# Kernel optimization log

Hardware: AMD Instinct MI355X
Metric: run time of the kernel (lower is better)

The kernel has to match this reference:

```python
import jax, jax.numpy as jnp
import numpy as np

N = 524288
L = 16            # encoding levels
F = 2             # features per level
LOG2_T = 19
T = 2 ** LOG2_T   # hash table size per level
BASE_RES = 16
FINEST = BASE_RES * 2 ** (L - 1)
WIDTH = 64
DENSITY_OUT = 16

# corner offsets of a voxel, i (x) outer, k (z) inner -- matches BOX_OFFSETS
OFFSETS = jnp.array([[i, j, k] for i in (0, 1) for j in (0, 1) for k in (0, 1)], dtype=jnp.int32)  # [8,3]
# primes wrapped to int32 exactly as jax x32 canonicalization does in the original
PRIMES = jnp.asarray(np.array([1, 2654435761, 805459861], dtype=np.int64).astype(np.int32))
_b = np.exp((np.log(FINEST) - np.log(BASE_RES)) / (L - 1))
RESOLUTIONS = jnp.asarray(np.floor(BASE_RES * _b ** np.arange(L)).astype(np.float32))  # [L]


def sh_encode(d):
    """Spherical harmonic encoding, degree 4 -> [N,25], faithful to source coeffs."""
    x, y, z = d[..., 0:1], d[..., 1:2], d[..., 2:3]
    x2, y2, z2 = x * x, y * y, z * z
    xy, xz, yz = x * y, x * z, y * z
    x4, y4 = x2 * x2, y2 * y2
    out = [jnp.full_like(x, 0.5 * np.sqrt(1.0 / np.pi))]
    c1 = 0.5 * np.sqrt(3.0 / np.pi)
    out += [-c1 * y, c1 * z, -c1 * x]
    sub = 0.25 * np.sqrt(5.0 / np.pi)
    v1 = 0.25 * np.sqrt(15.0 / np.pi)
    v2 = 0.5 * np.sqrt(15.0 / np.pi)
    v3 = 0.75 * np.sqrt(5.0 / np.pi)
    out += [v2 * xy, -v2 * yz, v3 * z2 - sub, -v2 * xz, v1 * x2 - v1 * y2]
    w1 = 0.25 * np.sqrt(105.0 / np.pi)
    w2 = 0.5 * np.sqrt(105.0 / np.pi)
    w3 = 0.25 * np.sqrt(35.0 / (2.0 * np.pi))
    w4 = 0.5 * np.sqrt(7.0 / (6.0 * np.pi))
    out += [-w3 * y * (3.0 * x2 - y2), w2 * xy * z, w4 * y * (1.5 - 7.5 * z2),
            1.24392110863372 * z * (1.5 * z2 - 0.5) - 0.497568443453487 * z,
            w4 * x * (1.5 - 7.5 * z2), w1 * z * (x2 - y2), -w3 * x * (x2 - 3.0 * y2)]
    out += [2.5033429417967 * xy * (x2 - y2),
            -1.77013076977993 * yz * (3.0 * x2 - y2),
            0.126156626101008 * xy * (52.5 * z2 - 7.5),
            0.267618617422916 * y * (2.33333333333333 * z * (1.5 - 7.5 * z2) + 4.0 * z),
            1.48099765681286 * z * (1.66666666666667 * z * (1.5 * z2 - 0.5) - 0.666666666666667 * z) - 0.952069922236839 * z2 + 0.317356640745613,
            0.267618617422916 * x * (2.33333333333333 * z * (1.5 - 7.5 * z2) + 4.0 * z),
            0.063078313050504 * (x2 - y2) * (52.5 * z2 - 7.5),
            -1.77013076977993 * xz * (x2 - 3.0 * y2),
            -3.75501441269506 * x2 * y2 + 0.625835735449176 * x4 + 0.625835735449176 * y4]
    return jnp.concatenate(out, axis=-1)  # [N,25]


def hash_grid_encode(x, tables):
    """x: [N,3] in unit cube; tables: [L,T,F] -> [N, L*F]."""
    def level(table, res):
        grid = 1.0 / res                              # box is [0,1]^3
        bl = jnp.floor(x / grid).astype(jnp.int32)    # bottom-left voxel index [N,3]
        w = (x - bl.astype(x.dtype) * grid) / grid    # trilinear weights [N,3]
        idx = bl[:, None, :] + OFFSETS[None]          # [N,8,3]
        h = ((idx[..., 0] * PRIMES[0]) ^ (idx[..., 1] * PRIMES[1]) ^ (idx[..., 2] * PRIMES[2])) % T
        emb = table[h]                                # [N,8,F] gather
        cw = jnp.where(OFFSETS[None].astype(bool), w[:, None, :], 1.0 - w[:, None, :]).prod(-1)  # [N,8]
        return jnp.einsum('ncf,nc->nf', emb, cw)
    feats = jax.vmap(level)(tables, RESOLUTIONS)      # [L,N,F]
    return jnp.transpose(feats, (1, 0, 2)).reshape(x.shape[0], L * F)


def setup_inputs() -> dict:
    key = jax.random.key(0)
    ks = jax.random.split(key, 8)
    position = jax.random.uniform(ks[0], (N, 3), jnp.float32)
    direction = jax.random.normal(ks[1], (N, 3), jnp.float32)
    hash_tables = jax.random.uniform(ks[2], (L, T, F), jnp.float32, -1e-4, 1e-4)
    def dense(k, fan_in, fan_out):
        return (jax.random.normal(k, (fan_in, fan_out), jnp.float32) / np.sqrt(fan_in),
                jnp.zeros((fan_out,), jnp.float32))
    W_d1, b_d1 = dense(ks[3], L * F, WIDTH)
    W_d2, b_d2 = dense(ks[4], WIDTH, DENSITY_OUT)
    W_c1, b_c1 = dense(ks[5], DENSITY_OUT + 25, WIDTH)
    W_c2, b_c2 = dense(ks[6], WIDTH, WIDTH)
    W_c3, b_c3 = dense(ks[7], WIDTH, 3)
    return dict(position=position, direction=direction, hash_tables=hash_tables,
                W_d1=W_d1, b_d1=b_d1, W_d2=W_d2, b_d2=b_d2,
                W_c1=W_c1, b_c1=b_c1, W_c2=W_c2, b_c2=b_c2, W_c3=W_c3, b_c3=b_c3)


def reference(position, direction, hash_tables, W_d1, b_d1, W_d2, b_d2,
              W_c1, b_c1, W_c2, b_c2, W_c3, b_c3):
    enc_pos = hash_grid_encode(position, hash_tables)     # [N,32]
    enc_dir = sh_encode(direction)                        # [N,25]
    y = jax.nn.relu(enc_pos @ W_d1 + b_d1)                # density MLP (1 hidden layer)
    density_out = y @ W_d2 + b_d2                         # [N,16]
    sigma = jax.nn.relu(density_out[:, -1:])              # [N,1]
    h = jnp.concatenate([density_out, enc_dir], axis=-1)  # [N,41]
    h = jax.nn.relu(h @ W_c1 + b_c1)
    h = jax.nn.relu(h @ W_c2 + b_c2)
    rgb = jax.nn.sigmoid(h @ W_c3 + b_c3)                 # [N,3]
    return (rgb, sigma)
```

## Files before the change

### kernel.cpp

```cpp
#include <hip/hip_runtime.h>
#include <math.h>

#define LEVELS 16
#define TBL 524288
#define TMASK (TBL - 1)

typedef short bf16x8 __attribute__((ext_vector_type(8)));
typedef float f32x4  __attribute__((ext_vector_type(4)));
typedef float fvec4  __attribute__((ext_vector_type(4)));
typedef unsigned int uvec4 __attribute__((ext_vector_type(4)));

static __device__ __forceinline__ unsigned short f2bf(float x) {
    unsigned u = __float_as_uint(x);
    u += 0x7fffu + ((u >> 16) & 1u);
    return (unsigned short)(u >> 16);
}
static __device__ __forceinline__ float b2f(unsigned short h) {
    return __uint_as_float(((unsigned)h) << 16);
}

#define SH_BLOCK(sh, dx, dy, dz)                                                          \
    const float x2 = dx * dx, y2 = dy * dy, z2 = dz * dz;                                 \
    const float xy = dx * dy, xz = dx * dz, yz = dy * dz;                                 \
    const float x4 = x2 * x2, y4 = y2 * y2;                                               \
    const float c0  = (float)(0.5 * sqrt(1.0 / M_PI));                                    \
    const float c1  = (float)(0.5 * sqrt(3.0 / M_PI));                                    \
    const float sub = (float)(0.25 * sqrt(5.0 / M_PI));                                   \
    const float v1  = (float)(0.25 * sqrt(15.0 / M_PI));                                  \
    const float v2  = (float)(0.5 * sqrt(15.0 / M_PI));                                   \
    const float v3  = (float)(0.75 * sqrt(5.0 / M_PI));                                   \
    const float w1c = (float)(0.25 * sqrt(105.0 / M_PI));                                 \
    const float w2c = (float)(0.5 * sqrt(105.0 / M_PI));                                  \
    const float w3c = (float)(0.25 * sqrt(35.0 / (2.0 * M_PI)));                          \
    const float w4c = (float)(0.5 * sqrt(7.0 / (6.0 * M_PI)));                            \
    sh[0] = c0;                                                                           \
    sh[1] = -c1 * dy;                                                                     \
    sh[2] =  c1 * dz;                                                                     \
    sh[3] = -c1 * dx;                                                                     \
    sh[4] =  v2 * xy;                                                                     \
    sh[5] = -v2 * yz;                                                                     \
    sh[6] =  v3 * z2 - sub;                                                               \
    sh[7] = -v2 * xz;                                                                     \
    sh[8] =  v1 * x2 - v1 * y2;                                                           \
    sh[9]  = -w3c * dy * (3.0f * x2 - y2);                                                \
    sh[10] =  w2c * xy * dz;                                                              \
    sh[11] =  w4c * dy * (1.5f - 7.5f * z2);                                              \
    sh[12] =  1.24392110863372f * dz * (1.5f * z2 - 0.5f) - 0.497568443453487f * dz;      \
    sh[13] =  w4c * dx * (1.5f - 7.5f * z2);                                              \
    sh[14] =  w1c * dz * (x2 - y2);                                                       \
    sh[15] = -w3c * dx * (x2 - 3.0f * y2);                                                \
    sh[16] =  2.5033429417967f * xy * (x2 - y2);                                          \
    sh[17] = -1.77013076977993f * yz * (3.0f * x2 - y2);                                  \
    sh[18] =  0.126156626101008f * xy * (52.5f * z2 - 7.5f);                              \
    sh[19] =  0.267618617422916f * dy * (2.33333333333333f * dz * (1.5f - 7.5f * z2) + 4.0f * dz); \
    sh[20] =  1.48099765681286f * dz * (1.66666666666667f * dz * (1.5f * z2 - 0.5f) - 0.666666666666667f * dz) \
              - 0.952069922236839f * z2 + 0.317356640745613f;                             \
    sh[21] =  0.267618617422916f * dx * (2.33333333333333f * dz * (1.5f - 7.5f * z2) + 4.0f * dz); \
    sh[22] =  0.063078313050504f * (x2 - y2) * (52.5f * z2 - 7.5f);                       \
    sh[23] = -1.77013076977993f * xz * (x2 - 3.0f * y2);                                  \
    sh[24] = -3.75501441269506f * x2 * y2 + 0.625835735449176f * x4 + 0.625835735449176f * y4;

__global__ __launch_bounds__(256)
void cvt_tables(const float* __restrict__ tables,
                unsigned int* __restrict__ tb16, int total)
{
    const int i = (blockIdx.x * 256 + threadIdx.x) * 4;
    if (i >= total) return;
    const fvec4 a = __builtin_nontemporal_load((const fvec4*)(tables + 2 * (size_t)i));
    const fvec4 b = __builtin_nontemporal_load((const fvec4*)(tables + 2 * (size_t)i) + 1);
    uvec4 o;
    o.x = ((unsigned)f2bf(a.y) << 16) | f2bf(a.x);
    o.y = ((unsigned)f2bf(a.w) << 16) | f2bf(a.z);
    o.z = ((unsigned)f2bf(b.y) << 16) | f2bf(b.x);
    o.w = ((unsigned)f2bf(b.w) << 16) | f2bf(b.z);
    __builtin_nontemporal_store(o, (uvec4*)&tb16[i]);
}

__global__ __launch_bounds__(256)
void ngp_encode_lvl(const float* __restrict__ pos,
                    const unsigned int* __restrict__ tb16,
                    unsigned int* __restrict__ wsp, int n)
{
    const int b = blockIdx.x;
    const int p = b & 7;
    const int h = b >> 14;
    const int l = 2 * p + h;
    const int c = (b & 16383) >> 3;
    const int idx = c * 256 + threadIdx.x;
    if (idx >= n || l >= LEVELS) return;

    const float px = pos[3 * idx + 0];
    const float py = pos[3 * idx + 1];
    const float pz = pos[3 * idx + 2];

    const float resf = (float)(16 << l);
    const float tx = px * resf, ty = py * resf, tz = pz * resf;
    const float fx = floorf(tx), fy = floorf(ty), fz = floorf(tz);
    const float wx = tx - fx, wy = ty - fy, wz = tz - fz;
    const unsigned ix = (unsigned)(int)fx;
    const unsigned iy = (unsigned)(int)fy;
    const unsigned iz = (unsigned)(int)fz;
    const unsigned hy0 = iy * 2654435761u, hy1 = hy0 + 2654435761u;
    const unsigned hz0 = iz * 805459861u,  hz1 = hz0 + 805459861u;
    const unsigned ix1 = ix + 1u;

    const unsigned int* tb = tb16 + (size_t)l * TBL;
    const unsigned hA = hy0 ^ hz0;
    const unsigned hB = hy0 ^ hz1;
    const unsigned hC = hy1 ^ hz0;
    const unsigned hD = hy1 ^ hz1;

    unsigned eA0, eA1, eB0, eB1, eC0, eC1, eD0, eD1;
    if ((ix & 1u) == 0u) {
        const uint2 pA = *(const uint2*)&tb[((ix ^ hA) & TMASK) & ~1u];
        const uint2 pB = *(const uint2*)&tb[((ix ^ hB) & TMASK) & ~1u];
        const uint2 pC = *(const uint2*)&tb[((ix ^ hC) & TMASK) & ~1u];
        const uint2 pD = *(const uint2*)&tb[((ix ^ hD) & TMASK) & ~1u];
        const unsigned sA = hA & 1u, sB = hB & 1u, sC = hC & 1u, sD = hD & 1u;
        eA0 = sA ? pA.y : pA.x;  eA1 = sA ? pA.x : pA.y;
        eB0 = sB ? pB.y : pB.x;  eB1 = sB ? pB.x : pB.y;
        eC0 = sC ? pC.y : pC.x;  eC1 = sC ? pC.x : pC.y;
        eD0 = sD ? pD.y : pD.x;  eD1 = sD ? pD.x : pD.y;
    } else {
        eA0 = tb[(ix  ^ hA) & TMASK];  eA1 = tb[(ix1 ^ hA) & TMASK];
        eB0 = tb[(ix  ^ hB) & TMASK];  eB1 = tb[(ix1 ^ hB) & TMASK];
        eC0 = tb[(ix  ^ hC) & TMASK];  eC1 = tb[(ix1 ^ hC) & TMASK];
        eD0 = tb[(ix  ^ hD) & TMASK];  eD1 = tb[(ix1 ^ hD) & TMASK];
    }

#define UNPX(e) __uint_as_float((e) << 16)
#define UNPY(e) __uint_as_float((e) & 0xffff0000u)

    const float ux = 1.f - wx, uy = 1.f - wy, uz = 1.f - wz;
    const float c000 = ux * uy * uz, c001 = ux * uy * wz;
    const float c010 = ux * wy * uz, c011 = ux * wy * wz;
    const float c100 = wx * uy * uz, c101 = wx * uy * wz;
    const float c110 = wx * wy * uz, c111 = wx * wy * wz;

    float f0 = UNPX(eA0) * c000, f1 = UNPY(eA0) * c000;
    f0 = fmaf(UNPX(eB0), c001, f0); f1 = fmaf(UNPY(eB0), c001, f1);
    f0 = fmaf(UNPX(eC0), c010, f0); f1 = fmaf(UNPY(eC0), c010, f1);
    f0 = fmaf(UNPX(eD0), c011, f0); f1 = fmaf(UNPY(eD0), c011, f1);
    f0 = fmaf(UNPX(eA1), c100, f0); f1 = fmaf(UNPY(eA1), c100, f1);
    f0 = fmaf(UNPX(eB1), c101, f0); f1 = fmaf(UNPY(eB1), c101, f1);
    f0 = fmaf(UNPX(eC1), c110, f0); f1 = fmaf(UNPY(eC1), c110, f1);
    f0 = fmaf(UNPX(eD1), c111, f0); f1 = fmaf(UNPY(eD1), c111, f1);

    const unsigned int h0 = f2bf(f0);
    const unsigned int h1 = f2bf(f1);
    __builtin_nontemporal_store((h1 << 16) | h0, &wsp[(size_t)l * n + idx]);
}

#define MT   512
#define GROUPS 8
#define SW1  32
#define SW   72
#define SA   65
#define OW1  0
#define OW2  2048
#define OC1H 3200
#define OC1L 7808
#define OC2H 12416
#define OC2L 17024
#define OC3H 21632
#define OC3L 22784
#define WTOT 23936

__global__ __launch_bounds__(512, 2)
void ngp_mlp_mfma4(const unsigned int* __restrict__ wsp,
                   const float* __restrict__ dirp,
                   const float* __restrict__ Wd1, const float* __restrict__ bd1,
                   const float* __restrict__ Wd2, const float* __restrict__ bd2,
                   const float* __restrict__ Wc1, const float* __restrict__ bc1,
                   const float* __restrict__ Wc2, const float* __restrict__ bc2,
                   const float* __restrict__ Wc3, const float* __restrict__ bc3,
                   float* __restrict__ out, int n)
{
    __shared__ short wsm[WTOT];
    __shared__ float act[8 * 16 * SA];
    const int tid = threadIdx.x;

    for (int t = tid; t < WTOT; t += MT) wsm[t] = 0;
    __syncthreads();

    for (int g = tid; g < 32 * 64; g += MT) {
        const int k = g >> 6, nn = g & 63;
        wsm[OW1 + nn * SW1 + k] = f2bf(Wd1[g]);
    }
    for (int g = tid; g < 64 * 16; g += MT) {
        const int k = g >> 4, nn = g & 15;
        wsm[OW2 + nn * SW + k] = f2bf(Wd2[g]);
    }
    for (int g = tid; g < 41 * 64; g += MT) {
        const int k = g >> 6, nn = g & 63;
        const float w = Wc1[g];
        const unsigned short hh = f2bf(w);
        wsm[OC1H + nn * SW + k] = hh;
        wsm[OC1L + nn * SW + k] = f2bf(w - b2f(hh));
    }
    for (int g = tid; g < 64 * 64; g += MT) {
        const int k = g >> 6, nn = g & 63;
        const float w = Wc2[g];
        const unsigned short hh = f2bf(w);
        wsm[OC2H + nn * SW + k] = hh;
        wsm[OC2L + nn * SW + k] = f2bf(w - b2f(hh));
    }
    for (int g = tid; g < 64 * 3; g += MT) {
        const int k = g / 3, nn = g - 3 * k;
        const float w = Wc3[g];
        const unsigned short hh = f2bf(w);
        wsm[OC3H + nn * SW + k] = hh;
        wsm[OC3L + nn * SW + k] = f2bf(w - b2f(hh));
    }
    __syncthreads();

    const int wid = tid >> 6;
    const int lane = tid & 63;
    const int ln = lane & 15;
    const int qd = lane >> 4;
    float* A = act + wid * (16 * SA);

    float bd1v[4], bc1v[4], bc2v[4];
#pragma unroll
    for (int t = 0; t < 4; ++t) {
        bd1v[t] = bd1[t * 16 + ln];
        bc1v[t] = bc1[t * 16 + ln];
        bc2v[t] = bc2[t * 16 + ln];
    }
    const float bd2v = bd2[ln];
    const float bc3v = (ln < 3) ? bc3[ln] : 0.f;

#define LOAD_SPLIT(ah, al, k0)                                   \
    {                                                            \
        _Pragma("unroll")                                        \
        for (int j = 0; j < 8; ++j) {                            \
            const float v = A[ln * SA + (k0) + j];               \
            const unsigned short hb = f2bf(v);                   \
            ah[j] = (short)hb;                                   \
            al[j] = (short)f2bf(v - b2f(hb));                    \
        }                                                        \
    }

#define SPLIT_TILE(acc, ah0, ah1, al0, al1, OH, OL, row)                                          \
    {                                                                                             \
        const bf16x8 bh0 = *(const bf16x8*)&wsm[(OH) + (row) * SW + qd * 8];                      \
        const bf16x8 bh1 = *(const bf16x8*)&wsm[(OH) + (row) * SW + 32 + qd * 8];                 \
        acc = __builtin_amdgcn_mfma_f32_16x16x32_bf16(ah0, bh0, acc, 0, 0, 0);                    \
        acc = __builtin_amdgcn_mfma_f32_16x16x32_bf16(ah1, bh1, acc, 0, 0, 0);                    \
        acc = __builtin_amdgcn_mfma_f32_16x16x32_bf16(al0, bh0, acc, 0, 0, 0);                    \
        acc = __builtin_amdgcn_mfma_f32_16x16x32_bf16(al1, bh1, acc, 0, 0, 0);                    \
        const bf16x8 bl0 = *(const bf16x8*)&wsm[(OL) + (row) * SW + qd * 8];                      \
        const bf16x8 bl1 = *(const bf16x8*)&wsm[(OL) + (row) * SW + 32 + qd * 8];                 \
        acc = __builtin_amdgcn_mfma_f32_16x16x32_bf16(ah0, bl0, acc, 0, 0, 0);                    \
        acc = __builtin_amdgcn_mfma_f32_16x16x32_bf16(ah1, bl1, acc, 0, 0, 0);                    \
    }

    const int pt0 = blockIdx.x * (GROUPS * 128) + wid * 16 + ln;
    unsigned int xu0, xu1, xu2, xu3;
    float dq0, dq1, dq2;
    xu0 = wsp[(size_t)(qd * 4 + 0) * n + pt0];
    xu1 = wsp[(size_t)(qd * 4 + 1) * n + pt0];
    xu2 = wsp[(size_t)(qd * 4 + 2) * n + pt0];
    xu3 = wsp[(size_t)(qd * 4 + 3) * n + pt0];
    dq0 = dirp[3 * pt0 + 0];
    dq1 = dirp[3 * pt0 + 1];
    dq2 = dirp[3 * pt0 + 2];

#pragma unroll 1
    for (int grp = 0; grp < GROUPS; ++grp) {
        const int pt_base = blockIdx.x * (GROUPS * 128) + grp * 128 + wid * 16;
        const int pt = pt_base + ln;

        bf16x8 ax;
        ax[0] = (short)(xu0 & 0xffffu); ax[1] = (short)(xu0 >> 16);
        ax[2] = (short)(xu1 & 0xffffu); ax[3] = (short)(xu1 >> 16);
        ax[4] = (short)(xu2 & 0xffffu); ax[5] = (short)(xu2 >> 16);
        ax[6] = (short)(xu3 & 0xffffu); ax[7] = (short)(xu3 >> 16);
        const float ddx = dq0, ddy = dq1, ddz = dq2;

        if (grp + 1 < GROUPS) {
            const int ptn = pt + 128;
            xu0 = wsp[(size_t)(qd * 4 + 0) * n + ptn];
            xu1 = wsp[(size_t)(qd * 4 + 1) * n + ptn];
            xu2 = wsp[(size_t)(qd * 4 + 2) * n + ptn];
            xu3 = wsp[(size_t)(qd * 4 + 3) * n + ptn];
            dq0 = dirp[3 * ptn + 0];
            dq1 = dirp[3 * ptn + 1];
            dq2 = dirp[3 * ptn + 2];
        }

        f32x4 yacc[4];
#pragma unroll
        for (int t = 0; t < 4; ++t) {
            const bf16x8 b = *(const bf16x8*)&wsm[OW1 + (t * 16 + ln) * SW1 + qd * 8];
            const float bv = bd1v[t];
            f32x4 acc = {bv, bv, bv, bv};
            yacc[t] = __builtin_amdgcn_mfma_f32_16x16x32_bf16(ax, b, acc, 0, 0, 0);
        }
#pragma unroll
        for (int t = 0; t < 4; ++t)
#pragma unroll
            for (int r = 0; r < 4; ++r)
                A[(qd * 4 + r) * SA + t * 16 + ln] = fmaxf(yacc[t][r], 0.f);

        {
            bf16x8 a0, a1;
#pragma unroll
            for (int j = 0; j < 8; ++j) a0[j] = (short)f2bf(A[ln * SA + qd * 8 + j]);
#pragma unroll
            for (int j = 0; j < 8; ++j) a1[j] = (short)f2bf(A[ln * SA + 32 + qd * 8 + j]);
            const bf16x8 b0 = *(const bf16x8*)&wsm[OW2 + ln * SW + qd * 8];
            const bf16x8 b1 = *(const bf16x8*)&wsm[OW2 + ln * SW + 32 + qd * 8];
            const float bv = bd2v;
            f32x4 acc = {bv, bv, bv, bv};
            acc = __builtin_amdgcn_mfma_f32_16x16x32_bf16(a0, b0, acc, 0, 0, 0);
            acc = __builtin_amdgcn_mfma_f32_16x16x32_bf16(a1, b1, acc, 0, 0, 0);
            if (ln == 15) {
#pragma unroll
                for (int r = 0; r < 4; ++r)
                    out[3 * n + pt_base + qd * 4 + r] = fmaxf(acc[r], 0.f);
            }
#pragma unroll
            for (int r = 0; r < 4; ++r)
                A[(qd * 4 + r) * SA + ln] = acc[r];
        }

        {
            float sh[25];
            SH_BLOCK(sh, ddx, ddy, ddz)
#pragma unroll
            for (int i = 0; i < 25; ++i)
                if ((i & 3) == qd)
                    A[ln * SA + 16 + i] = sh[i];
        }

        {
            bf16x8 ah0, ah1, al0, al1;
            LOAD_SPLIT(ah0, al0, qd * 8)
            LOAD_SPLIT(ah1, al1, 32 + qd * 8)
            f32x4 hacc[4];
#pragma unroll
            for (int t = 0; t < 4; ++t) {
                const float bv = bc1v[t];
                f32x4 acc = {bv, bv, bv, bv};
                SPLIT_TILE(acc, ah0, ah1, al0, al1, OC1H, OC1L, t * 16 + ln)
                hacc[t] = acc;
            }
#pragma unroll
            for (int t = 0; t < 4; ++t)
#pragma unroll
                for (int r = 0; r < 4; ++r)
                    A[(qd * 4 + r) * SA + t * 16 + ln] = fmaxf(hacc[t][r], 0.f);
        }

        {
            bf16x8 ah0, ah1, al0, al1;
            LOAD_SPLIT(ah0, al0, qd * 8)
            LOAD_SPLIT(ah1, al1, 32 + qd * 8)
            f32x4 hacc[4];
#pragma unroll
            for (int t = 0; t < 4; ++t) {
                const float bv = bc2v[t];
                f32x4 acc = {bv, bv, bv, bv};
                SPLIT_TILE(acc, ah0, ah1, al0, al1, OC2H, OC2L, t * 16 + ln)
                hacc[t] = acc;
            }
#pragma unroll
            for (int t = 0; t < 4; ++t)
#pragma unroll
                for (int r = 0; r < 4; ++r)
                    A[(qd * 4 + r) * SA + t * 16 + ln] = fmaxf(hacc[t][r], 0.f);
        }

        {
            bf16x8 ah0, ah1, al0, al1;
            LOAD_SPLIT(ah0, al0, qd * 8)
            LOAD_SPLIT(ah1, al1, 32 + qd * 8)
            const float bv = bc3v;
            f32x4 acc = {bv, bv, bv, bv};
            SPLIT_TILE(acc, ah0, ah1, al0, al1, OC3H, OC3L, ln)
            if (ln < 3) {
#pragma unroll
                for (int r = 0; r < 4; ++r)
                    out[3 * (pt_base + qd * 4 + r) + ln] = 1.f / (1.f + expf(-acc[r]));
            }
        }
    }
}

__global__ __launch_bounds__(256)
void nerf_fused(const float* __restrict__ pos,
                const float* __restrict__ dirp,
                const float* __restrict__ tables,
                const float* __restrict__ Wd1, const float* __restrict__ bd1,
                const float* __restrict__ Wd2, const float* __restrict__ bd2,
                const float* __restrict__ Wc1, const float* __restrict__ bc1,
                const float* __restrict__ Wc2, const float* __restrict__ bc2,
                const float* __restrict__ Wc3, const float* __restrict__ bc3,
                float* __restrict__ out, int n)
{
    const int idx = blockIdx.x * blockDim.x + threadIdx.x;
    if (idx >= n) return;
    const float px = pos[3 * idx + 0], py = pos[3 * idx + 1], pz = pos[3 * idx + 2];
    float y[64];
#pragma unroll
    for (int j = 0; j < 64; ++j) y[j] = bd1[j];
#pragma unroll
    for (int l = 0; l < LEVELS; ++l) {
        const float resf = (float)(16 << l);
        const float tx = px * resf, ty = py * resf, tz = pz * resf;
        const float fx = floorf(tx), fy = floorf(ty), fz = floorf(tz);
        const float wx = tx - fx, wy = ty - fy, wz = tz - fz;
        const unsigned ix = (unsigned)(int)fx, iy = (unsigned)(int)fy, iz = (unsigned)(int)fz;
        const unsigned hy0 = iy * 2654435761u, hy1 = hy0 + 2654435761u;
        const unsigned hz0 = iz * 805459861u,  hz1 = hz0 + 805459861u;
        const unsigned ix1 = ix + 1u;
        const float2* tb = (const float2*)tables + (size_t)l * TBL;
        const float2 e000 = tb[(ix  ^ hy0 ^ hz0) & TMASK];
        const float2 e001 = tb[(ix  ^ hy0 ^ hz1) & TMASK];
        const float2 e010 = tb[(ix  ^ hy1 ^ hz0) & TMASK];
        const float2 e011 = tb[(ix  ^ hy1 ^ hz1) & TMASK];
        const float2 e100 = tb[(ix1 ^ hy0 ^ hz0) & TMASK];
        const float2 e101 = tb[(ix1 ^ hy0 ^ hz1) & TMASK];
        const float2 e110 = tb[(ix1 ^ hy1 ^ hz0) & TMASK];
        const float2 e111 = tb[(ix1 ^ hy1 ^ hz1) & TMASK];
        const float ux = 1.f - wx, uy = 1.f - wy, uz = 1.f - wz;
        const float c000 = ux*uy*uz, c001 = ux*uy*wz, c010 = ux*wy*uz, c011 = ux*wy*wz;
        const float c100 = wx*uy*uz, c101 = wx*uy*wz, c110 = wx*wy*uz, c111 = wx*wy*wz;
        float f0 = e000.x*c000, f1 = e000.y*c000;
        f0 = fmaf(e001.x,c001,f0); f1 = fmaf(e001.y,c001,f1);
        f0 = fmaf(e010.x,c010,f0); f1 = fmaf(e010.y,c010,f1);
        f0 = fmaf(e011.x,c011,f0); f1 = fmaf(e011.y,c011,f1);
        f0 = fmaf(e100.x,c100,f0); f1 = fmaf(e100.y,c100,f1);
        f0 = fmaf(e101.x,c101,f0); f1 = fmaf(e101.y,c101,f1);
        f0 = fmaf(e110.x,c110,f0); f1 = fmaf(e110.y,c110,f1);
        f0 = fmaf(e111.x,c111,f0); f1 = fmaf(e111.y,c111,f1);
        const float* w0 = Wd1 + (size_t)(2 * l) * 64;
#pragma unroll
        for (int j = 0; j < 64; ++j)
            y[j] = fmaf(f0, w0[j], fmaf(f1, w0[64 + j], y[j]));
    }
    float d[16];
#pragma unroll
    for (int k = 0; k < 16; ++k) d[k] = bd2[k];
#pragma unroll
    for (int j = 0; j < 64; ++j) {
        const float a = fmaxf(y[j], 0.f);
#pragma unroll
        for (int k = 0; k < 16; ++k) d[k] = fmaf(a, Wd2[j * 16 + k], d[k]);
    }
    out[3 * n + idx] = fmaxf(d[15], 0.f);
    const float dx = dirp[3*idx], dy = dirp[3*idx+1], dz = dirp[3*idx+2];
    float sh[25];
    SH_BLOCK(sh, dx, dy, dz)
    float h1[64];
#pragma unroll
    for (int j = 0; j < 64; ++j) h1[j] = bc1[j];
#pragma unroll
    for (int i = 0; i < 16; ++i) {
#pragma unroll
        for (int j = 0; j < 64; ++j) h1[j] = fmaf(d[i], Wc1[i * 64 + j], h1[j]);
    }
#pragma unroll
    for (int s = 0; s < 25; ++s) {
#pragma unroll
        for (int j = 0; j < 64; ++j) h1[j] = fmaf(sh[s], Wc1[(16 + s) * 64 + j], h1[j]);
    }
    float h2[64];
#pragma unroll
    for (int j = 0; j < 64; ++j) h2[j] = bc2[j];
#pragma unroll
    for (int i = 0; i < 64; ++i) {
        const float a = fmaxf(h1[i], 0.f);
#pragma unroll
        for (int j = 0; j < 64; ++j) h2[j] = fmaf(a, Wc2[i * 64 + j], h2[j]);
    }
    float r0 = bc3[0], r1 = bc3[1], r2 = bc3[2];
#pragma unroll
    for (int j = 0; j < 64; ++j) {
        const float a = fmaxf(h2[j], 0.f);
        r0 = fmaf(a, Wc3[j * 3 + 0], r0);
        r1 = fmaf(a, Wc3[j * 3 + 1], r1);
        r2 = fmaf(a, Wc3[j * 3 + 2], r2);
    }
    out[3 * idx + 0] = 1.f / (1.f + expf(-r0));
    out[3 * idx + 1] = 1.f / (1.f + expf(-r1));
    out[3 * idx + 2] = 1.f / (1.f + expf(-r2));
}

extern "C" void kernel_launch(void* const* d_in, const int* in_sizes, int n_in,
                              void* d_out, int out_size, void* d_ws, size_t ws_size,
                              hipStream_t stream) {
    const float* pos    = (const float*)d_in[0];
    const float* dir    = (const float*)d_in[1];
    const float* tables = (const float*)d_in[2];
    const float* Wd1 = (const float*)d_in[3];
    const float* bd1 = (const float*)d_in[4];
    const float* Wd2 = (const float*)d_in[5];
    const float* bd2 = (const float*)d_in[6];
    const float* Wc1 = (const float*)d_in[7];
    const float* bc1 = (const float*)d_in[8];
    const float* Wc2 = (const float*)d_in[9];
    const float* bc2 = (const float*)d_in[10];
    const float* Wc3 = (const float*)d_in[11];
    const float* bc3 = (const float*)d_in[12];

    const int n = in_sizes[0] / 3;
    const int blocks = (n + 255) / 256;

    if (ws_size >= (size_t)n * 128 && n == 524288) {
        unsigned int* wsp  = (unsigned int*)d_ws;
        unsigned int* tb16 = (unsigned int*)((char*)d_ws + (size_t)n * 64);
        const int total = LEVELS * TBL;
        cvt_tables<<<total / 1024, 256, 0, stream>>>(tables, tb16, total);
        ngp_encode_lvl<<<16 * blocks, 256, 0, stream>>>(pos, tb16, wsp, n);
        ngp_mlp_mfma4<<<n / (128 * GROUPS), MT, 0, stream>>>((const unsigned int*)wsp, dir,
                                                             Wd1, bd1, Wd2, bd2,
                                                             Wc1, bc1, Wc2, bc2, Wc3, bc3,
                                                             (float*)d_out, n);
    } else {
        nerf_fused<<<blocks, 256, 0, stream>>>(pos, dir, tables,
                                               Wd1, bd1, Wd2, bd2,
                                               Wc1, bc1, Wc2, bc2, Wc3, bc3,
                                               (float*)d_out, n);
    }
}
```

Baseline: 360.7 us.

## Process two 16-point tiles per wave in MLP and split encode launches

The MLP kernel moves from 512 to 256 threads per block, with each wave now handling two 16-point tiles (A and B) so every B-operand weight fragment loaded from shared memory feeds twice as many MFMAs. It also emits SH coefficients directly into the activation buffer, pads the activation stride from 65 to 68, shrinks the Wc3 weight region (rows indexed by ln&3), and adds sched_barriers between output tiles. The level-encode launch is split into two launches of eight levels each, replacing the old interleaved block-to-level mapping. The costs are higher register pressure per wave, which could hurt occupancy, and one extra kernel launch.

```diff
diff --git a/kernel.cpp b/kernel.cpp
--- a/kernel.cpp
+++ b/kernel.cpp
@@ -60,6 +60,49 @@
     sh[23] = -1.77013076977993f * xz * (x2 - 3.0f * y2);                                  \
     sh[24] = -3.75501441269506f * x2 * y2 + 0.625835735449176f * x4 + 0.625835735449176f * y4;
 
+#define SH_EMIT(Ash, DXV, DYV, DZV)                                                        \
+    {                                                                                      \
+        const float sx2 = (DXV)*(DXV), sy2 = (DYV)*(DYV), sz2 = (DZV)*(DZV);               \
+        const float sxy = (DXV)*(DYV), sxz = (DXV)*(DZV), syz = (DYV)*(DZV);               \
+        const float sx4 = sx2*sx2, sy4 = sy2*sy2;                                          \
+        const float k0  = (float)(0.5 * sqrt(1.0 / M_PI));                                 \
+        const float k1  = (float)(0.5 * sqrt(3.0 / M_PI));                                 \
+        const float ksub= (float)(0.25 * sqrt(5.0 / M_PI));                                \
+        const float kv1 = (float)(0.25 * sqrt(15.0 / M_PI));                               \
+        const float kv2 = (float)(0.5 * sqrt(15.0 / M_PI));                                \
+        const float kv3 = (float)(0.75 * sqrt(5.0 / M_PI));                                \
+        const float kw1 = (float)(0.25 * sqrt(105.0 / M_PI));                              \
+        const float kw2 = (float)(0.5 * sqrt(105.0 / M_PI));                               \
+        const float kw3 = (float)(0.25 * sqrt(35.0 / (2.0 * M_PI)));                       \
+        const float kw4 = (float)(0.5 * sqrt(7.0 / (6.0 * M_PI)));                         \
+        if ((0  & 3) == qd) (Ash)[0]  = k0;                                                \
+        if ((1  & 3) == qd) (Ash)[1]  = -k1 * (DYV);                                       \
+        if ((2  & 3) == qd) (Ash)[2]  =  k1 * (DZV);                                       \
+        if ((3  & 3) == qd) (Ash)[3]  = -k1 * (DXV);                                       \
+        if ((4  & 3) == qd) (Ash)[4]  =  kv2 * sxy;                                        \
+        if ((5  & 3) == qd) (Ash)[5]  = -kv2 * syz;                                        \
+        if ((6  & 3) == qd) (Ash)[6]  =  kv3 * sz2 - ksub;                                 \
+        if ((7  & 3) == qd) (Ash)[7]  = -kv2 * sxz;                                        \
+        if ((8  & 3) == qd) (Ash)[8]  =  kv1 * sx2 - kv1 * sy2;                            \
+        if ((9  & 3) == qd) (Ash)[9]  = -kw3 * (DYV) * (3.0f * sx2 - sy2);                 \
+        if ((10 & 3) == qd) (Ash)[10] =  kw2 * sxy * (DZV);                                \
+        if ((11 & 3) == qd) (Ash)[11] =  kw4 * (DYV) * (1.5f - 7.5f * sz2);                \
+        if ((12 & 3) == qd) (Ash)[12] =  1.24392110863372f * (DZV) * (1.5f * sz2 - 0.5f) - 0.497568443453487f * (DZV); \
+        if ((13 & 3) == qd) (Ash)[13] =  kw4 * (DXV) * (1.5f - 7.5f * sz2);                \
+        if ((14 & 3) == qd) (Ash)[14] =  kw1 * (DZV) * (sx2 - sy2);                        \
+        if ((15 & 3) == qd) (Ash)[15] = -kw3 * (DXV) * (sx2 - 3.0f * sy2);                 \
+        if ((16 & 3) == qd) (Ash)[16] =  2.5033429417967f * sxy * (sx2 - sy2);             \
+        if ((17 & 3) == qd) (Ash)[17] = -1.77013076977993f * syz * (3.0f * sx2 - sy2);     \
+        if ((18 & 3) == qd) (Ash)[18] =  0.126156626101008f * sxy * (52.5f * sz2 - 7.5f);  \
+        if ((19 & 3) == qd) (Ash)[19] =  0.267618617422916f * (DYV) * (2.33333333333333f * (DZV) * (1.5f - 7.5f * sz2) + 4.0f * (DZV)); \
+        if ((20 & 3) == qd) (Ash)[20] =  1.48099765681286f * (DZV) * (1.66666666666667f * (DZV) * (1.5f * sz2 - 0.5f) - 0.666666666666667f * (DZV)) \
+                                         - 0.952069922236839f * sz2 + 0.317356640745613f;  \
+        if ((21 & 3) == qd) (Ash)[21] =  0.267618617422916f * (DXV) * (2.33333333333333f * (DZV) * (1.5f - 7.5f * sz2) + 4.0f * (DZV)); \
+        if ((22 & 3) == qd) (Ash)[22] =  0.063078313050504f * (sx2 - sy2) * (52.5f * sz2 - 7.5f); \
+        if ((23 & 3) == qd) (Ash)[23] = -1.77013076977993f * sxz * (sx2 - 3.0f * sy2);     \
+        if ((24 & 3) == qd) (Ash)[24] = -3.75501441269506f * sx2 * sy2 + 0.625835735449176f * sx4 + 0.625835735449176f * sy4; \
+    }
+
 __global__ __launch_bounds__(256)
 void cvt_tables(const float* __restrict__ tables,
                 unsigned int* __restrict__ tb16, int total)
@@ -79,13 +122,11 @@
 __global__ __launch_bounds__(256)
 void ngp_encode_lvl(const float* __restrict__ pos,
                     const unsigned int* __restrict__ tb16,
-                    unsigned int* __restrict__ wsp, int n)
+                    unsigned int* __restrict__ wsp, int n, int lbase)
 {
     const int b = blockIdx.x;
-    const int p = b & 7;
-    const int h = b >> 14;
-    const int l = 2 * p + h;
-    const int c = (b & 16383) >> 3;
+    const int l = lbase + (b & 7);
+    const int c = b >> 3;
     const int idx = c * 256 + threadIdx.x;
     if (idx >= n || l >= LEVELS) return;
 
@@ -151,11 +192,10 @@
     __builtin_nontemporal_store((h1 << 16) | h0, &wsp[(size_t)l * n + idx]);
 }
 
-#define MT   512
 #define GROUPS 8
 #define SW1  32
 #define SW   72
-#define SA   65
+#define SA   68
 #define OW1  0
 #define OW2  2048
 #define OC1H 3200
@@ -163,10 +203,10 @@
 #define OC2H 12416
 #define OC2L 17024
 #define OC3H 21632
-#define OC3L 22784
-#define WTOT 23936
-
-__global__ __launch_bounds__(512, 2)
+#define OC3L 21920
+#define WTOT 22208
+
+__global__ __launch_bounds__(256, 2)
 void ngp_mlp_mfma4(const unsigned int* __restrict__ wsp,
                    const float* __restrict__ dirp,
                    const float* __restrict__ Wd1, const float* __restrict__ bd1,
@@ -177,35 +217,35 @@
                    float* __restrict__ out, int n)
 {
     __shared__ short wsm[WTOT];
-    __shared__ float act[8 * 16 * SA];
+    __shared__ float act[4 * 32 * SA];
     const int tid = threadIdx.x;
 
-    for (int t = tid; t < WTOT; t += MT) wsm[t] = 0;
+    for (int t = tid; t < WTOT; t += 256) wsm[t] = 0;
     __syncthreads();
 
-    for (int g = tid; g < 32 * 64; g += MT) {
+    for (int g = tid; g < 32 * 64; g += 256) {
         const int k = g >> 6, nn = g & 63;
         wsm[OW1 + nn * SW1 + k] = f2bf(Wd1[g]);
     }
-    for (int g = tid; g < 64 * 16; g += MT) {
+    for (int g = tid; g < 64 * 16; g += 256) {
         const int k = g >> 4, nn = g & 15;
         wsm[OW2 + nn * SW + k] = f2bf(Wd2[g]);
     }
-    for (int g = tid; g < 41 * 64; g += MT) {
+    for (int g = tid; g < 41 * 64; g += 256) {
         const int k = g >> 6, nn = g & 63;
         const float w = Wc1[g];
         const unsigned short hh = f2bf(w);
         wsm[OC1H + nn * SW + k] = hh;
         wsm[OC1L + nn * SW + k] = f2bf(w - b2f(hh));
     }
-    for (int g = tid; g < 64 * 64; g += MT) {
+    for (int g = tid; g < 64 * 64; g += 256) {
         const int k = g >> 6, nn = g & 63;
         const float w = Wc2[g];
         const unsigned short hh = f2bf(w);
         wsm[OC2H + nn * SW + k] = hh;
         wsm[OC2L + nn * SW + k] = f2bf(w - b2f(hh));
     }
-    for (int g = tid; g < 64 * 3; g += MT) {
+    for (int g = tid; g < 64 * 3; g += 256) {
         const int k = g / 3, nn = g - 3 * k;
         const float w = Wc3[g];
         const unsigned short hh = f2bf(w);
@@ -218,7 +258,8 @@
     const int lane = tid & 63;
     const int ln = lane & 15;
     const int qd = lane >> 4;
-    float* A = act + wid * (16 * SA);
+    float* A0 = act + wid * (32 * SA);
+    float* A1 = A0 + 16 * SA;
 
     float bd1v[4], bc1v[4], bc2v[4];
 #pragma unroll
@@ -230,159 +271,199 @@
     const float bd2v = bd2[ln];
     const float bc3v = (ln < 3) ? bc3[ln] : 0.f;
 
-#define LOAD_SPLIT(ah, al, k0)                                   \
+#define LOAD_SPLITP(AP, ah, al, k0)                              \
     {                                                            \
         _Pragma("unroll")                                        \
         for (int j = 0; j < 8; ++j) {                            \
-            const float v = A[ln * SA + (k0) + j];               \
+            const float v = (AP)[ln * SA + (k0) + j];            \
             const unsigned short hb = f2bf(v);                   \
             ah[j] = (short)hb;                                   \
             al[j] = (short)f2bf(v - b2f(hb));                    \
         }                                                        \
     }
 
-#define SPLIT_TILE(acc, ah0, ah1, al0, al1, OH, OL, row)                                          \
+#define SPLIT_TILE2(accA, accB, hA0, hA1, lA0, lA1, hB0, hB1, lB0, lB1, OH, OL, row)              \
     {                                                                                             \
         const bf16x8 bh0 = *(const bf16x8*)&wsm[(OH) + (row) * SW + qd * 8];                      \
         const bf16x8 bh1 = *(const bf16x8*)&wsm[(OH) + (row) * SW + 32 + qd * 8];                 \
-        acc = __builtin_amdgcn_mfma_f32_16x16x32_bf16(ah0, bh0, acc, 0, 0, 0);                    \
-        acc = __builtin_amdgcn_mfma_f32_16x16x32_bf16(ah1, bh1, acc, 0, 0, 0);                    \
-        acc = __builtin_amdgcn_mfma_f32_16x16x32_bf16(al0, bh0, acc, 0, 0, 0);                    \
-        acc = __builtin_amdgcn_mfma_f32_16x16x32_bf16(al1, bh1, acc, 0, 0, 0);                    \
+        accA = __builtin_amdgcn_mfma_f32_16x16x32_bf16(hA0, bh0, accA, 0, 0, 0);                  \
+        accA = __builtin_amdgcn_mfma_f32_16x16x32_bf16(hA1, bh1, accA, 0, 0, 0);                  \
+        accA = __builtin_amdgcn_mfma_f32_16x16x32_bf16(lA0, bh0, accA, 0, 0, 0);                  \
+        accA = __builtin_amdgcn_mfma_f32_16x16x32_bf16(lA1, bh1, accA, 0, 0, 0);                  \
+        accB = __builtin_amdgcn_mfma_f32_16x16x32_bf16(hB0, bh0, accB, 0, 0, 0);                  \
+        accB = __builtin_amdgcn_mfma_f32_16x16x32_bf16(hB1, bh1, accB, 0, 0, 0);                  \
+        accB = __builtin_amdgcn_mfma_f32_16x16x32_bf16(lB0, bh0, accB, 0, 0, 0);                  \
+        accB = __builtin_amdgcn_mfma_f32_16x16x32_bf16(lB1, bh1, accB, 0, 0, 0);                  \
         const bf16x8 bl0 = *(const bf16x8*)&wsm[(OL) + (row) * SW + qd * 8];                      \
         const bf16x8 bl1 = *(const bf16x8*)&wsm[(OL) + (row) * SW + 32 + qd * 8];                 \
-        acc = __builtin_amdgcn_mfma_f32_16x16x32_bf16(ah0, bl0, acc, 0, 0, 0);                    \
-        acc = __builtin_amdgcn_mfma_f32_16x16x32_bf16(ah1, bl1, acc, 0, 0, 0);                    \
-    }
-
-    const int pt0 = blockIdx.x * (GROUPS * 128) + wid * 16 + ln;
-    unsigned int xu0, xu1, xu2, xu3;
-    float dq0, dq1, dq2;
-    xu0 = wsp[(size_t)(qd * 4 + 0) * n + pt0];
-    xu1 = wsp[(size_t)(qd * 4 + 1) * n + pt0];
-    xu2 = wsp[(size_t)(qd * 4 + 2) * n + pt0];
-    xu3 = wsp[(size_t)(qd * 4 + 3) * n + pt0];
-    dq0 = dirp[3 * pt0 + 0];
-    dq1 = dirp[3 * pt0 + 1];
-    dq2 = dirp[3 * pt0 + 2];
+        accA = __builtin_amdgcn_mfma_f32_16x16x32_bf16(hA0, bl0, accA, 0, 0, 0);                  \
+        accA = __builtin_amdgcn_mfma_f32_16x16x32_bf16(hA1, bl1, accA, 0, 0, 0);                  \
+        accB = __builtin_amdgcn_mfma_f32_16x16x32_bf16(hB0, bl0, accB, 0, 0, 0);                  \
+        accB = __builtin_amdgcn_mfma_f32_16x16x32_bf16(hB1, bl1, accB, 0, 0, 0);                  \
+    }
+
+    const int ptA0 = blockIdx.x * (GROUPS * 128) + wid * 32 + ln;
+    unsigned int xuA0, xuA1, xuA2, xuA3, xuB0, xuB1, xuB2, xuB3;
+    float dqA0, dqA1, dqA2, dqB0, dqB1, dqB2;
+    xuA0 = wsp[(size_t)(qd * 4 + 0) * n + ptA0];
+    xuA1 = wsp[(size_t)(qd * 4 + 1) * n + ptA0];
+    xuA2 = wsp[(size_t)(qd * 4 + 2) * n + ptA0];
+    xuA3 = wsp[(size_t)(qd * 4 + 3) * n + ptA0];
+    xuB0 = wsp[(size_t)(qd * 4 + 0) * n + ptA0 + 16];
+    xuB1 = wsp[(size_t)(qd * 4 + 1) * n + ptA0 + 16];
+    xuB2 = wsp[(size_t)(qd * 4 + 2) * n + ptA0 + 16];
+    xuB3 = wsp[(size_t)(qd * 4 + 3) * n + ptA0 + 16];
+    dqA0 = dirp[3 * ptA0 + 0];
+    dqA1 = dirp[3 * ptA0 + 1];
+    dqA2 = dirp[3 * ptA0 + 2];
+    dqB0 = dirp[3 * (ptA0 + 16) + 0];
+    dqB1 = dirp[3 * (ptA0 + 16) + 1];
+    dqB2 = dirp[3 * (ptA0 + 16) + 2];
 
 #pragma unroll 1
     for (int grp = 0; grp < GROUPS; ++grp) {
-        const int pt_base = blockIdx.x * (GROUPS * 128) + grp * 128 + wid * 16;
+        const int pt_base = blockIdx.x * (GROUPS * 128) + grp * 128 + wid * 32;
         const int pt = pt_base + ln;
 
-        bf16x8 ax;
-        ax[0] = (short)(xu0 & 0xffffu); ax[1] = (short)(xu0 >> 16);
-        ax[2] = (short)(xu1 & 0xffffu); ax[3] = (short)(xu1 >> 16);
-        ax[4] = (short)(xu2 & 0xffffu); ax[5] = (short)(xu2 >> 16);
-        ax[6] = (short)(xu3 & 0xffffu); ax[7] = (short)(xu3 >> 16);
-        const float ddx = dq0, ddy = dq1, ddz = dq2;
+        bf16x8 axA, axB;
+        axA[0] = (short)(xuA0 & 0xffffu); axA[1] = (short)(xuA0 >> 16);
+        axA[2] = (short)(xuA1 & 0xffffu); axA[3] = (short)(xuA1 >> 16);
+        axA[4] = (short)(xuA2 & 0xffffu); axA[5] = (short)(xuA2 >> 16);
+        axA[6] = (short)(xuA3 & 0xffffu); axA[7] = (short)(xuA3 >> 16);
+        axB[0] = (short)(xuB0 & 0xffffu); axB[1] = (short)(xuB0 >> 16);
+        axB[2] = (short)(xuB1 & 0xffffu); axB[3] = (short)(xuB1 >> 16);
+        axB[4] = (short)(xuB2 & 0xffffu); axB[5] = (short)(xuB2 >> 16);
+        axB[6] = (short)(xuB3 & 0xffffu); axB[7] = (short)(xuB3 >> 16);
+        const float dAx = dqA0, dAy = dqA1, dAz = dqA2;
+        const float dBx = dqB0, dBy = dqB1, dBz = dqB2;
 
         if (grp + 1 < GROUPS) {
             const int ptn = pt + 128;
-            xu0 = wsp[(size_t)(qd * 4 + 0) * n + ptn];
-            xu1 = wsp[(size_t)(qd * 4 + 1) * n + ptn];
-            xu2 = wsp[(size_t)(qd * 4 + 2) * n + ptn];
-            xu3 = wsp[(size_t)(qd * 4 + 3) * n + ptn];
-            dq0 = dirp[3 * ptn + 0];
-            dq1 = dirp[3 * ptn + 1];
-            dq2 = dirp[3 * ptn + 2];
+            xuA0 = wsp[(size_t)(qd * 4 + 0) * n + ptn];
+            xuA1 = wsp[(size_t)(qd * 4 + 1) * n + ptn];
+            xuA2 = wsp[(size_t)(qd * 4 + 2) * n + ptn];
+            xuA3 = wsp[(size_t)(qd * 4 + 3) * n + ptn];
+            xuB0 = wsp[(size_t)(qd * 4 + 0) * n + ptn + 16];
+            xuB1 = wsp[(size_t)(qd * 4 + 1) * n + ptn + 16];
+            xuB2 = wsp[(size_t)(qd * 4 + 2) * n + ptn + 16];
+            xuB3 = wsp[(size_t)(qd * 4 + 3) * n + ptn + 16];
+            dqA0 = dirp[3 * ptn + 0];
+            dqA1 = dirp[3 * ptn + 1];
+            dqA2 = dirp[3 * ptn + 2];
+            dqB0 = dirp[3 * (ptn + 16) + 0];
+            dqB1 = dirp[3 * (ptn + 16) + 1];
+            dqB2 = dirp[3 * (ptn + 16) + 2];
         }
 
-        f32x4 yacc[4];
 #pragma unroll
         for (int t = 0; t < 4; ++t) {
             const bf16x8 b = *(const bf16x8*)&wsm[OW1 + (t * 16 + ln) * SW1 + qd * 8];
             const float bv = bd1v[t];
-            f32x4 acc = {bv, bv, bv, bv};
-            yacc[t] = __builtin_amdgcn_mfma_f32_16x16x32_bf16(ax, b, acc, 0, 0, 0);
+            f32x4 accA = {bv, bv, bv, bv};
+            f32x4 accB = {bv, bv, bv, bv};
+            accA = __builtin_amdgcn_mfma_f32_16x16x32_bf16(axA, b, accA, 0, 0, 0);
+            accB = __builtin_amdgcn_mfma_f32_16x16x32_bf16(axB, b, accB, 0, 0, 0);
+#pragma unroll
+            for (int r = 0; r < 4; ++r) {
+                A0[(qd * 4 + r) * SA + t * 16 + ln] = fmaxf(accA[r], 0.f);
+                A1[(qd * 4 + r) * SA + t * 16 + ln] = fmaxf(accB[r], 0.f);
+            }
         }
-#pragma unroll
-        for (int t = 0; t < 4; ++t)
-#pragma unroll
-            for (int r = 0; r < 4; ++r)
-                A[(qd * 4 + r) * SA + t * 16 + ln] = fmaxf(yacc[t][r], 0.f);
 
         {
-            bf16x8 a0, a1;
-#pragma unroll
-            for (int j = 0; j < 8; ++j) a0[j] = (short)f2bf(A[ln * SA + qd * 8 + j]);
-#pragma unroll
-            for (int j = 0; j < 8; ++j) a1[j] = (short)f2bf(A[ln * SA + 32 + qd * 8 + j]);
+            bf16x8 a0A, a1A, a0B, a1B;
+#pragma unroll
+            for (int j = 0; j < 8; ++j) a0A[j] = (short)f2bf(A0[ln * SA + qd * 8 + j]);
+#pragma unroll
+            for (int j = 0; j < 8; ++j) a1A[j] = (short)f2bf(A0[ln * SA + 32 + qd * 8 + j]);
+#pragma unroll
+            for (int j = 0; j < 8; ++j) a0B[j] = (short)f2bf(A1[ln * SA + qd * 8 + j]);
+#pragma unroll
+            for (int j = 0; j < 8; ++j) a1B[j] = (short)f2bf(A1[ln * SA + 32 + qd * 8 + j]);
             const bf16x8 b0 = *(const bf16x8*)&wsm[OW2 + ln * SW + qd * 8];
             const bf16x8 b1 = *(const bf16x8*)&wsm[OW2 + ln * SW + 32 + qd * 8];
             const float bv = bd2v;
-            f32x4 acc = {bv, bv, bv, bv};
-            acc = __builtin_amdgcn_mfma_f32_16x16x32_bf16(a0, b0, acc, 0, 0, 0);
-            acc = __builtin_amdgcn_mfma_f32_16x16x32_bf16(a1, b1, acc, 0, 0, 0);
+            f32x4 accA = {bv, bv, bv, bv};
+            f32x4 accB = {bv, bv, bv, bv};
+            accA = __builtin_amdgcn_mfma_f32_16x16x32_bf16(a0A, b0, accA, 0, 0, 0);
+            accA = __builtin_amdgcn_mfma_f32_16x16x32_bf16(a1A, b1, accA, 0, 0, 0);
+            accB = __builtin_amdgcn_mfma_f32_16x16x32_bf16(a0B, b0, accB, 0, 0, 0);
+            accB = __builtin_amdgcn_mfma_f32_16x16x32_bf16(a1B, b1, accB, 0, 0, 0);
             if (ln == 15) {
 #pragma unroll
-                for (int r = 0; r < 4; ++r)
-                    out[3 * n + pt_base + qd * 4 + r] = fmaxf(acc[r], 0.f);
+                for (int r = 0; r < 4; ++r) {
+                    out[3 * n + pt_base + qd * 4 + r]      = fmaxf(accA[r], 0.f);
+                    out[3 * n + pt_base + 16 + qd * 4 + r] = fmaxf(accB[r], 0.f);
+                }
             }
 #pragma unroll
-            for (int r = 0; r < 4; ++r)
-                A[(qd * 4 + r) * SA + ln] = acc[r];
+            for (int r = 0; r < 4; ++r) {
+                A0[(qd * 4 + r) * SA + ln] = accA[r];
+                A1[(qd * 4 + r) * SA + ln] = accB[r];
+            }
         }
 
+        SH_EMIT(&A0[ln * SA + 16], dAx, dAy, dAz)
+        SH_EMIT(&A1[ln * SA + 16], dBx, dBy, dBz)
+
         {
-            float sh[25];
-            SH_BLOCK(sh, ddx, ddy, ddz)
-#pragma unroll
-            for (int i = 0; i < 25; ++i)
-                if ((i & 3) == qd)
-                    A[ln * SA + 16 + i] = sh[i];
-        }
-
-        {
-            bf16x8 ah0, ah1, al0, al1;
-            LOAD_SPLIT(ah0, al0, qd * 8)
-            LOAD_SPLIT(ah1, al1, 32 + qd * 8)
-            f32x4 hacc[4];
+            bf16x8 hA0, hA1, lA0, lA1, hB0, hB1, lB0, lB1;
+            LOAD_SPLITP(A0, hA0, lA0, qd * 8)
+            LOAD_SPLITP(A0, hA1, lA1, 32 + qd * 8)
+            LOAD_SPLITP(A1, hB0, lB0, qd * 8)
+            LOAD_SPLITP(A1, hB1, lB1, 32 + qd * 8)
 #pragma unroll
             for (int t = 0; t < 4; ++t) {
                 const float bv = bc1v[t];
-                f32x4 acc = {bv, bv, bv, bv};
-                SPLIT_TILE(acc, ah0, ah1, al0, al1, OC1H, OC1L, t * 16 + ln)
-                hacc[t] = acc;
+                f32x4 accA = {bv, bv, bv, bv};
+                f32x4 accB = {bv, bv, bv, bv};
+                SPLIT_TILE2(accA, accB, hA0, hA1, lA0, lA1, hB0, hB1, lB0, lB1, OC1H, OC1L, t * 16 + ln)
+#pragma unroll
+                for (int r = 0; r < 4; ++r) {
+                    A0[(qd * 4 + r) * SA + t * 16 + ln] = fmaxf(accA[r], 0.f);
+                    A1[(qd * 4 + r) * SA + t * 16 + ln] = fmaxf(accB[r], 0.f);
+                }
+                __builtin_amdgcn_sched_barrier(0);
             }
-#pragma unroll
-            for (int t = 0; t < 4; ++t)
-#pragma unroll
-                for (int r = 0; r < 4; ++r)
-                    A[(qd * 4 + r) * SA + t * 16 + ln] = fmaxf(hacc[t][r], 0.f);
         }
 
         {
-            bf16x8 ah0, ah1, al0, al1;
-            LOAD_SPLIT(ah0, al0, qd * 8)
-            LOAD_SPLIT(ah1, al1, 32 + qd * 8)
-            f32x4 hacc[4];
+            bf16x8 hA0, hA1, lA0, lA1, hB0, hB1, lB0, lB1;
+            LOAD_SPLITP(A0, hA0, lA0, qd * 8)
+            LOAD_SPLITP(A0, hA1, lA1, 32 + qd * 8)
+            LOAD_SPLITP(A1, hB0, lB0, qd * 8)
+            LOAD_SPLITP(A1, hB1, lB1, 32 + qd * 8)
 #pragma unroll
             for (int t = 0; t < 4; ++t) {
                 const float bv = bc2v[t];
-                f32x4 acc = {bv, bv, bv, bv};
-                SPLIT_TILE(acc, ah0, ah1, al0, al1, OC2H, OC2L, t * 16 + ln)
-                hacc[t] = acc;
+                f32x4 accA = {bv, bv, bv, bv};
+                f32x4 accB = {bv, bv, bv, bv};
+                SPLIT_TILE2(accA, accB, hA0, hA1, lA0, lA1, hB0, hB1, lB0, lB1, OC2H, OC2L, t * 16 + ln)
+#pragma unroll
+                for (int r = 0; r < 4; ++r) {
+                    A0[(qd * 4 + r) * SA + t * 16 + ln] = fmaxf(accA[r], 0.f);
+                    A1[(qd * 4 + r) * SA + t * 16 + ln] = fmaxf(accB[r], 0.f);
+                }
+                __builtin_amdgcn_sched_barrier(0);
             }
-#pragma unroll
-            for (int t = 0; t < 4; ++t)
-#pragma unroll
-                for (int r = 0; r < 4; ++r)
-                    A[(qd * 4 + r) * SA + t * 16 + ln] = fmaxf(hacc[t][r], 0.f);
         }
 
         {
-            bf16x8 ah0, ah1, al0, al1;
-            LOAD_SPLIT(ah0, al0, qd * 8)
-            LOAD_SPLIT(ah1, al1, 32 + qd * 8)
+            bf16x8 hA0, hA1, lA0, lA1, hB0, hB1, lB0, lB1;
+            LOAD_SPLITP(A0, hA0, lA0, qd * 8)
+            LOAD_SPLITP(A0, hA1, lA1, 32 + qd * 8)
+            LOAD_SPLITP(A1, hB0, lB0, qd * 8)
+            LOAD_SPLITP(A1, hB1, lB1, 32 + qd * 8)
             const float bv = bc3v;
-            f32x4 acc = {bv, bv, bv, bv};
-            SPLIT_TILE(acc, ah0, ah1, al0, al1, OC3H, OC3L, ln)
+            f32x4 accA = {bv, bv, bv, bv};
+            f32x4 accB = {bv, bv, bv, bv};
+            SPLIT_TILE2(accA, accB, hA0, hA1, lA0, lA1, hB0, hB1, lB0, lB1, OC3H, OC3L, (ln & 3))
             if (ln < 3) {
 #pragma unroll
-                for (int r = 0; r < 4; ++r)
-                    out[3 * (pt_base + qd * 4 + r) + ln] = 1.f / (1.f + expf(-acc[r]));
+                for (int r = 0; r < 4; ++r) {
+                    out[3 * (pt_base + qd * 4 + r) + ln]      = 1.f / (1.f + expf(-accA[r]));
+                    out[3 * (pt_base + 16 + qd * 4 + r) + ln] = 1.f / (1.f + expf(-accB[r]));
+                }
             }
         }
     }
@@ -513,11 +594,12 @@
         unsigned int* tb16 = (unsigned int*)((char*)d_ws + (size_t)n * 64);
         const int total = LEVELS * TBL;
         cvt_tables<<<total / 1024, 256, 0, stream>>>(tables, tb16, total);
-        ngp_encode_lvl<<<16 * blocks, 256, 0, stream>>>(pos, tb16, wsp, n);
-        ngp_mlp_mfma4<<<n / (128 * GROUPS), MT, 0, stream>>>((const unsigned int*)wsp, dir,
-                                                             Wd1, bd1, Wd2, bd2,
-                                                             Wc1, bc1, Wc2, bc2, Wc3, bc3,
-                                                             (float*)d_out, n);
+        ngp_encode_lvl<<<8 * blocks, 256, 0, stream>>>(pos, tb16, wsp, n, 0);
+        ngp_encode_lvl<<<8 * blocks, 256, 0, stream>>>(pos, tb16, wsp, n, 8);
+        ngp_mlp_mfma4<<<n / (GROUPS * 128), 256, 0, stream>>>((const unsigned int*)wsp, dir,
+                                                              Wd1, bd1, Wd2, bd2,
+                                                              Wc1, bc1, Wc2, bc2, Wc3, bc3,
+                                                              (float*)d_out, n);
     } else {
         nerf_fused<<<blocks, 256, 0, stream>>>(pos, dir, tables,
                                                Wd1, bd1, Wd2, bd2,
```

Measured after the change: 355.2 us. Within noise of the previous version (-1.5%).
